# Kernel tuning notes

Measured on AMD Instinct MI355X. Metric: run time of the kernel, lower is better.

The kernel has to match this reference:

```python
import jax, jax.numpy as jnp
import numpy as np

N_NODES = 100000
N_EDGES = 3200000
D = 16
L = 3


def setup_inputs() -> dict:
    key = jax.random.key(0)
    ks = jax.random.split(key, 7)
    scale = 1.0 / np.sqrt(D)
    x = jax.random.normal(ks[0], (N_NODES, D), dtype=jnp.float32)
    edge_index = jax.random.randint(ks[1], (2, N_EDGES), 0, N_NODES, dtype=jnp.int64)
    Wl = jax.random.normal(ks[2], (L, D, D), dtype=jnp.float32) * scale
    bl = jax.random.normal(ks[3], (L, D), dtype=jnp.float32) * scale
    Wr = jax.random.normal(ks[4], (L, D, D), dtype=jnp.float32) * scale
    Wlin = jax.random.normal(ks[5], (L, D, D), dtype=jnp.float32) * scale
    blin = jax.random.normal(ks[6], (L, D), dtype=jnp.float32) * scale
    return {"x": x, "edge_index": edge_index, "Wl": Wl, "bl": bl,
            "Wr": Wr, "Wlin": Wlin, "blin": blin}


def reference(x, edge_index, Wl, bl, Wr, Wlin, blin):
    src = edge_index[0]
    dst = edge_index[1]
    n = x.shape[0]
    # in-degree for mean aggregation (PyG SAGEConv aggr='mean')
    deg = jax.ops.segment_sum(jnp.ones((src.shape[0],), dtype=x.dtype), dst,
                              num_segments=n)
    denom = jnp.maximum(deg, 1.0)[:, None]  # nodes with no in-edges -> 0 agg
    for i in range(Wl.shape[0]):
        # gather source features, scatter-mean onto targets
        agg = jax.ops.segment_sum(x[src], dst, num_segments=n) / denom
        conv = agg @ Wl[i].T + bl[i] + x @ Wr[i].T  # SAGEConv: lin_l(agg)+lin_r(x)
        x = conv + x @ Wlin[i].T + blin[i]          # + Linear residual
    return x
```

## Files before the change

kernel.cpp:

```cpp
#include <hip/hip_runtime.h>

#define N_NODES 100000
#define N_EDGES 3200000
#define D 16

#define TILE 128
#define NB ((N_NODES + TILE - 1) / TILE)
#define CAP 4608
#define NBLK 500
#define SEG (N_EDGES / NBLK)
#define BINT 1024
#define CVTB 391
#define LT 512
#define N4 (N_NODES * D / 4)

__device__ __forceinline__ unsigned packbf(float a, float b) {
    unsigned ua = __float_as_uint(a); ua += 0x7FFFu + ((ua >> 16) & 1u);
    unsigned ub = __float_as_uint(b); ub += 0x7FFFu + ((ub >> 16) & 1u);
    return (ua >> 16) | (ub & 0xFFFF0000u);
}
#define BLO(u) __uint_as_float((u) << 16)
#define BHI(u) __uint_as_float((u) & 0xFFFF0000u)

__global__ __launch_bounds__(BINT, 8) void pre_kernel(
        const float* __restrict__ x, unsigned* __restrict__ xbf,
        const int* __restrict__ src, const int* __restrict__ dst,
        int* __restrict__ cursor, unsigned* __restrict__ ebuf) {
    __shared__ int lcnt[NB];
    __shared__ int ldiff[NB];
    __shared__ unsigned sorted[SEG];
    __shared__ unsigned short sbkt[SEG];
    __shared__ int wsum[16];
    int tid = threadIdx.x;

    if (blockIdx.x >= NBLK) {
        int t = (blockIdx.x - NBLK) * BINT + tid;
        if (t < N4) {
            float4 v = *(const float4*)(x + (size_t)t * 4);
            uint2 o; o.x = packbf(v.x, v.y); o.y = packbf(v.z, v.w);
            *(uint2*)(xbf + (size_t)t * 2) = o;
        }
        return;
    }

    for (int i = tid; i < NB; i += BINT) lcnt[i] = 0;
    __syncthreads();
    int b0 = blockIdx.x * SEG;
    for (int e = b0 + tid * 4; e < b0 + SEG; e += BINT * 4) {
        int4 d4 = *(const int4*)(dst + e);
        atomicAdd(&lcnt[d4.x >> 7], 1);
        atomicAdd(&lcnt[d4.y >> 7], 1);
        atomicAdd(&lcnt[d4.z >> 7], 1);
        atomicAdd(&lcnt[d4.w >> 7], 1);
    }
    __syncthreads();
    {
        int lane = tid & 63, wv = tid >> 6;
        int v = (tid < NB) ? lcnt[tid] : 0;
        int s = v;
        #pragma unroll
        for (int d_ = 1; d_ < 64; d_ <<= 1) {
            int u = __shfl_up(s, d_, 64);
            if (lane >= d_) s += u;
        }
        if (lane == 63) wsum[wv] = s;
        __syncthreads();
        if (tid == 0) {
            int a = 0;
            #pragma unroll
            for (int i = 0; i < 16; i++) { int t_ = wsum[i]; wsum[i] = a; a += t_; }
        }
        __syncthreads();
        int excl = wsum[wv] + s - v;
        if (tid < NB) {
            int g = v ? (tid * CAP + atomicAdd(&cursor[tid], v)) : 0;
            ldiff[tid] = g - excl;
            lcnt[tid] = excl;
        }
        __syncthreads();
    }
    for (int e = b0 + tid * 4; e < b0 + SEG; e += BINT * 4) {
        int4 d4 = *(const int4*)(dst + e);
        int4 s4 = *(const int4*)(src + e);
        int b_, pos;
        b_ = d4.x >> 7; pos = atomicAdd(&lcnt[b_], 1);
        sorted[pos] = ((unsigned)(d4.x & 127) << 17) | (unsigned)s4.x; sbkt[pos] = (unsigned short)b_;
        b_ = d4.y >> 7; pos = atomicAdd(&lcnt[b_], 1);
        sorted[pos] = ((unsigned)(d4.y & 127) << 17) | (unsigned)s4.y; sbkt[pos] = (unsigned short)b_;
        b_ = d4.z >> 7; pos = atomicAdd(&lcnt[b_], 1);
        sorted[pos] = ((unsigned)(d4.z & 127) << 17) | (unsigned)s4.z; sbkt[pos] = (unsigned short)b_;
        b_ = d4.w >> 7; pos = atomicAdd(&lcnt[b_], 1);
        sorted[pos] = ((unsigned)(d4.w & 127) << 17) | (unsigned)s4.w; sbkt[pos] = (unsigned short)b_;
    }
    __syncthreads();
    for (int i = tid; i < SEG; i += BINT) {
        int b_ = sbkt[i];
        ebuf[ldiff[b_] + i] = sorted[i];
    }
}

#define LDG(j) (*(const uint4*)(xbf + (size_t)(se2[(j) + lane2] & 0x1FFFF) * 8 + ho))
#define LDC(j) (*(const uint4*)(xbf + (size_t)(se2[min((j) + lane2, s1m1)] & 0x1FFFF) * 8 + ho))
#define ACC8(g) do { \
    acc[0] += BLO((g).x); acc[1] += BHI((g).x); acc[2] += BLO((g).y); acc[3] += BHI((g).y); \
    acc[4] += BLO((g).z); acc[5] += BHI((g).z); acc[6] += BLO((g).w); acc[7] += BHI((g).w); } while (0)
#define ACC8M(g, m) do { \
    acc[0] = fmaf((m), BLO((g).x), acc[0]); acc[1] = fmaf((m), BHI((g).x), acc[1]); \
    acc[2] = fmaf((m), BLO((g).y), acc[2]); acc[3] = fmaf((m), BHI((g).y), acc[3]); \
    acc[4] = fmaf((m), BLO((g).z), acc[4]); acc[5] = fmaf((m), BHI((g).z), acc[5]); \
    acc[6] = fmaf((m), BLO((g).w), acc[6]); acc[7] = fmaf((m), BHI((g).w), acc[7]); } while (0)

__device__ __forceinline__ void agg_xform(
    const float* __restrict__ xin, const unsigned* __restrict__ xbf,
    const unsigned* se2, const int* lofs, int n_loc,
    const float* sWl, const float* sWc, const float* sbc,
    float* __restrict__ xout, unsigned* __restrict__ xbf_out,
    int emit_bf, int b, int N, int tid) {
    int q = tid & 3;
    int n = b * TILE + n_loc;
    if (n >= N) return;

    float4 xq = *(const float4*)(xin + (size_t)n * D + q * 4);
    float xv[4] = { xq.x, xq.y, xq.z, xq.w };

    int s0 = lofs[n_loc];
    int s1 = lofs[n_loc + 1];
    int deg = s1 - s0;
    int lane2 = q >> 1;
    int ho = (q & 1) * 4;

    float acc[8] = {0.f,0.f,0.f,0.f,0.f,0.f,0.f,0.f};
    int end8 = s0 + (deg & ~7);
    int i = s0;
    if (i < end8) {
        uint4 c0 = LDG(i + 0), c1 = LDG(i + 2), c2 = LDG(i + 4), c3 = LDG(i + 6);
        i += 8;
        for (; i < end8; i += 8) {
            uint4 n0 = LDG(i + 0), n1 = LDG(i + 2), n2 = LDG(i + 4), n3 = LDG(i + 6);
            ACC8(c0); ACC8(c1); ACC8(c2); ACC8(c3);
            c0 = n0; c1 = n1; c2 = n2; c3 = n3;
        }
        ACC8(c0); ACC8(c1); ACC8(c2); ACC8(c3);
    }
    if (i < s1) {
        int s1m1 = s1 - 1;
        int j0 = i + lane2;
        float m0 = (j0 + 0 < s1) ? 1.f : 0.f;
        float m1 = (j0 + 2 < s1) ? 1.f : 0.f;
        float m2 = (j0 + 4 < s1) ? 1.f : 0.f;
        float m3 = (j0 + 6 < s1) ? 1.f : 0.f;
        uint4 e0 = LDC(i + 0), e1 = LDC(i + 2), e2 = LDC(i + 4), e3 = LDC(i + 6);
        ACC8M(e0, m0); ACC8M(e1, m1); ACC8M(e2, m2); ACC8M(e3, m3);
    }
    #pragma unroll
    for (int k = 0; k < 8; k++) acc[k] += __shfl_xor(acc[k], 2, 4);

    int srcAbs = (tid & 63 & ~3) | (q >> 1);
    float inv = 1.0f / fmaxf((float)deg, 1.0f);
    float a[4];
    #pragma unroll
    for (int k = 0; k < 4; k++) {
        float lo = __shfl(acc[k], srcAbs);
        float hi = __shfl(acc[4 + k], srcAbs);
        a[k] = ((q & 1) ? hi : lo) * inv;
    }

    float o[4];
    #pragma unroll
    for (int j = 0; j < D; j++) {
        float p = 0.f;
        #pragma unroll
        for (int k = 0; k < 4; k++) {
            int kk = q * 4 + k;
            p += a[k] * sWl[j * D + kk] + xv[k] * sWc[j * D + kk];
        }
        p += __shfl_xor(p, 1, 4);
        p += __shfl_xor(p, 2, 4);
        if ((j >> 2) == q) o[j & 3] = p + sbc[j];
    }
    *(float4*)(xout + (size_t)n * D + q * 4) = make_float4(o[0], o[1], o[2], o[3]);
    if (emit_bf) {
        uint2 ob; ob.x = packbf(o[0], o[1]); ob.y = packbf(o[2], o[3]);
        *(uint2*)(xbf_out + (size_t)n * 8 + q * 2) = ob;
    }
}

__global__ void layer0_kernel(
        const float* __restrict__ xin, const unsigned* __restrict__ xbf,
        unsigned* __restrict__ ebuf, const int* __restrict__ cnt,
        int* __restrict__ node_start, int* __restrict__ gperm,
        const float* __restrict__ Wl, const float* __restrict__ bl,
        const float* __restrict__ Wr, const float* __restrict__ Wlin,
        const float* __restrict__ blin,
        float* __restrict__ xout, unsigned* __restrict__ xbf_out, int N) {
    __shared__ unsigned se[CAP];
    __shared__ unsigned se2[CAP];
    __shared__ int lcnt[TILE];
    __shared__ int lofs[TILE + 1];
    __shared__ int sdeg[TILE];
    __shared__ int perm[TILE];
    __shared__ float sWl[D * D];
    __shared__ float sWc[D * D];
    __shared__ float sbc[D];

    int tid = threadIdx.x;
    int b = blockIdx.x;
    int base = b * CAP;
    int nE = min(cnt[b], CAP);
    int nE4 = (nE + 3) >> 2;

    if (tid < D * D) { sWl[tid] = Wl[tid]; sWc[tid] = Wr[tid] + Wlin[tid]; }
    if (tid < D) sbc[tid] = bl[tid] + blin[tid];
    if (tid < TILE) lcnt[tid] = 0;
    for (int i = tid; i < nE4; i += LT)
        ((uint4*)se)[i] = ((const uint4*)(ebuf + base))[i];
    __syncthreads();
    for (int i = tid; i < nE; i += LT)
        atomicAdd(&lcnt[se[i] >> 17], 1);
    __syncthreads();
    if (tid < 64) {
        int l2 = tid * 2;
        int c0 = lcnt[l2], c1 = lcnt[l2 + 1];
        int v = c0 + c1, s = v;
        #pragma unroll
        for (int d_ = 1; d_ < 64; d_ <<= 1) {
            int u = __shfl_up(s, d_, 64);
            if (tid >= d_) s += u;
        }
        int excl = s - v;
        lofs[l2] = excl; sdeg[l2] = c0; lcnt[l2] = excl;
        node_start[b * TILE + l2] = excl;
        int e1 = excl + c0;
        lofs[l2 + 1] = e1; sdeg[l2 + 1] = c1; lcnt[l2 + 1] = e1;
        node_start[b * TILE + l2 + 1] = e1;
        if (tid == 63) lofs[TILE] = s;
    }
    __syncthreads();
    if (tid < TILE) {
        int dm = sdeg[tid];
        int r = 0;
        for (int j = 0; j < TILE; j++) {
            int dj = sdeg[j];
            r += (dj > dm) || (dj == dm && j < tid);
        }
        perm[r] = tid;
        gperm[b * TILE + r] = tid;
    }
    for (int i = tid; i < nE; i += LT) {
        unsigned p = se[i];
        int pos = atomicAdd(&lcnt[p >> 17], 1);
        se2[pos] = p;
    }
    __syncthreads();
    for (int i = tid; i < nE4; i += LT)
        ((uint4*)(ebuf + base))[i] = ((const uint4*)se2)[i];

    agg_xform(xin, xbf, se2, lofs, perm[tid >> 2], sWl, sWc, sbc,
              xout, xbf_out, 1, b, N, tid);
}

__global__ __launch_bounds__(LT, 8) void layerN_kernel(
        const float* __restrict__ xin, const unsigned* __restrict__ xbf,
        const unsigned* __restrict__ ebuf, const int* __restrict__ cnt,
        const int* __restrict__ node_start, const int* __restrict__ gperm,
        const float* __restrict__ Wl, const float* __restrict__ bl,
        const float* __restrict__ Wr, const float* __restrict__ Wlin,
        const float* __restrict__ blin,
        float* __restrict__ xout, unsigned* __restrict__ xbf_out,
        int emit_bf, int N) {
    __shared__ unsigned se2[CAP];
    __shared__ int lofs[TILE + 1];
    __shared__ float sWl[D * D];
    __shared__ float sWc[D * D];
    __shared__ float sbc[D];

    int tid = threadIdx.x;
    int b = blockIdx.x;
    int base = b * CAP;
    int nE = min(cnt[b], CAP);
    int nE4 = (nE + 3) >> 2;

    if (tid < D * D) { sWl[tid] = Wl[tid]; sWc[tid] = Wr[tid] + Wlin[tid]; }
    if (tid < D) sbc[tid] = bl[tid] + blin[tid];
    if (tid < TILE) lofs[tid] = node_start[b * TILE + tid];
    if (tid == 0) lofs[TILE] = nE;
    for (int i = tid; i < nE4; i += LT)
        ((uint4*)se2)[i] = ((const uint4*)(ebuf + base))[i];
    int n_loc = gperm[b * TILE + (tid >> 2)];
    __syncthreads();

    agg_xform(xin, xbf, se2, lofs, n_loc, sWl, sWc, sbc,
              xout, xbf_out, emit_bf, b, N, tid);
}

extern "C" void kernel_launch(void* const* d_in, const int* in_sizes, int n_in,
                              void* d_out, int out_size, void* d_ws, size_t ws_size,
                              hipStream_t stream) {
    const float* x    = (const float*)d_in[0];
    const int*   ei   = (const int*)d_in[1];
    const float* Wl   = (const float*)d_in[2];
    const float* bl   = (const float*)d_in[3];
    const float* Wr   = (const float*)d_in[4];
    const float* Wlin = (const float*)d_in[5];
    const float* blin = (const float*)d_in[6];
    float* out = (float*)d_out;

    const int* src = ei;
    const int* dst = ei + N_EDGES;

    char* w = (char*)d_ws;
    unsigned* ebuf   = (unsigned*)w;  w += (size_t)NB * CAP * 4;
    float* bufA      = (float*)w;     w += (size_t)N_NODES * D * 4;
    float* bufB      = (float*)w;     w += (size_t)N_NODES * D * 4;
    unsigned* xbf0   = (unsigned*)w;  w += (size_t)N_NODES * 8 * 4;
    unsigned* xbf1   = (unsigned*)w;  w += (size_t)N_NODES * 8 * 4;
    int*   cursor    = (int*)w;       w += (size_t)NB * 4;
    int*   node_start= (int*)w;       w += (size_t)NB * TILE * 4;
    int*   gperm     = (int*)w;       w += (size_t)NB * TILE * 4;

    hipMemsetAsync(cursor, 0, (size_t)NB * 4, stream);
    pre_kernel<<<NBLK + CVTB, BINT, 0, stream>>>(x, xbf0, src, dst, cursor, ebuf);

    layer0_kernel<<<NB, LT, 0, stream>>>(
        x, xbf0, ebuf, cursor, node_start, gperm,
        Wl, bl, Wr, Wlin, blin, bufA, xbf1, N_NODES);
    layerN_kernel<<<NB, LT, 0, stream>>>(
        bufA, xbf1, ebuf, cursor, node_start, gperm,
        Wl + D * D, bl + D, Wr + D * D, Wlin + D * D, blin + D, bufB, xbf0, 1, N_NODES);
    layerN_kernel<<<NB, LT, 0, stream>>>(
        bufB, xbf0, ebuf, cursor, node_start, gperm,
        Wl + 2 * D * D, bl + 2 * D, Wr + 2 * D * D, Wlin + 2 * D * D, blin + 2 * D,
        out, nullptr, 0, N_NODES);
}
```

Baseline: 188.9 us.

## Halve node tile to 64, fold bf16 conversion into bucketing blocks, drop layer0 staging buffer

Shrinks the destination-node tile from 128 to 64 nodes, which doubles the bucket count to 1563 and cuts per-block edge capacity and threads to 256. The pre-kernel scan now handles two buckets per thread, and the separate bf16-conversion blocks are merged into the 500 bucketing blocks. layer0 reads edges straight from global memory twice instead of staging them in a second shared array, halving its shared memory. The smaller blocks should raise occupancy and balance load, at the cost of more blocks and a higher overflow risk from the tighter CAP.

```diff
diff --git a/kernel.cpp b/kernel.cpp
--- a/kernel.cpp
+++ b/kernel.cpp
@@ -4,14 +4,13 @@
 #define N_EDGES 3200000
 #define D 16
 
-#define TILE 128
+#define TILE 64
 #define NB ((N_NODES + TILE - 1) / TILE)
-#define CAP 4608
+#define CAP 2432
 #define NBLK 500
 #define SEG (N_EDGES / NBLK)
 #define BINT 1024
-#define CVTB 391
-#define LT 512
+#define LT 256
 #define N4 (N_NODES * D / 4)
 
 __device__ __forceinline__ unsigned packbf(float a, float b) {
@@ -33,14 +32,13 @@
     __shared__ int wsum[16];
     int tid = threadIdx.x;
 
-    if (blockIdx.x >= NBLK) {
-        int t = (blockIdx.x - NBLK) * BINT + tid;
+    {
+        int t = blockIdx.x * BINT + tid;
         if (t < N4) {
             float4 v = *(const float4*)(x + (size_t)t * 4);
             uint2 o; o.x = packbf(v.x, v.y); o.y = packbf(v.z, v.w);
             *(uint2*)(xbf + (size_t)t * 2) = o;
         }
-        return;
     }
 
     for (int i = tid; i < NB; i += BINT) lcnt[i] = 0;
@@ -48,16 +46,18 @@
     int b0 = blockIdx.x * SEG;
     for (int e = b0 + tid * 4; e < b0 + SEG; e += BINT * 4) {
         int4 d4 = *(const int4*)(dst + e);
-        atomicAdd(&lcnt[d4.x >> 7], 1);
-        atomicAdd(&lcnt[d4.y >> 7], 1);
-        atomicAdd(&lcnt[d4.z >> 7], 1);
-        atomicAdd(&lcnt[d4.w >> 7], 1);
+        atomicAdd(&lcnt[d4.x >> 6], 1);
+        atomicAdd(&lcnt[d4.y >> 6], 1);
+        atomicAdd(&lcnt[d4.z >> 6], 1);
+        atomicAdd(&lcnt[d4.w >> 6], 1);
     }
     __syncthreads();
     {
         int lane = tid & 63, wv = tid >> 6;
-        int v = (tid < NB) ? lcnt[tid] : 0;
-        int s = v;
+        int i2 = tid * 2;
+        int c0 = (i2 < NB) ? lcnt[i2] : 0;
+        int c1 = (i2 + 1 < NB) ? lcnt[i2 + 1] : 0;
+        int v = c0 + c1, s = v;
         #pragma unroll
         for (int d_ = 1; d_ < 64; d_ <<= 1) {
             int u = __shfl_up(s, d_, 64);
@@ -72,10 +72,16 @@
         }
         __syncthreads();
         int excl = wsum[wv] + s - v;
-        if (tid < NB) {
-            int g = v ? (tid * CAP + atomicAdd(&cursor[tid], v)) : 0;
-            ldiff[tid] = g - excl;
-            lcnt[tid] = excl;
+        if (i2 < NB) {
+            int g = c0 ? (i2 * CAP + atomicAdd(&cursor[i2], c0)) : 0;
+            ldiff[i2] = g - excl;
+            lcnt[i2] = excl;
+        }
+        if (i2 + 1 < NB) {
+            int e1 = excl + c0;
+            int g = c1 ? ((i2 + 1) * CAP + atomicAdd(&cursor[i2 + 1], c1)) : 0;
+            ldiff[i2 + 1] = g - e1;
+            lcnt[i2 + 1] = e1;
         }
         __syncthreads();
     }
@@ -83,14 +89,14 @@
         int4 d4 = *(const int4*)(dst + e);
         int4 s4 = *(const int4*)(src + e);
         int b_, pos;
-        b_ = d4.x >> 7; pos = atomicAdd(&lcnt[b_], 1);
-        sorted[pos] = ((unsigned)(d4.x & 127) << 17) | (unsigned)s4.x; sbkt[pos] = (unsigned short)b_;
-        b_ = d4.y >> 7; pos = atomicAdd(&lcnt[b_], 1);
-        sorted[pos] = ((unsigned)(d4.y & 127) << 17) | (unsigned)s4.y; sbkt[pos] = (unsigned short)b_;
-        b_ = d4.z >> 7; pos = atomicAdd(&lcnt[b_], 1);
-        sorted[pos] = ((unsigned)(d4.z & 127) << 17) | (unsigned)s4.z; sbkt[pos] = (unsigned short)b_;
-        b_ = d4.w >> 7; pos = atomicAdd(&lcnt[b_], 1);
-        sorted[pos] = ((unsigned)(d4.w & 127) << 17) | (unsigned)s4.w; sbkt[pos] = (unsigned short)b_;
+        b_ = d4.x >> 6; pos = atomicAdd(&lcnt[b_], 1);
+        sorted[pos] = ((unsigned)(d4.x & 63) << 17) | (unsigned)s4.x; sbkt[pos] = (unsigned short)b_;
+        b_ = d4.y >> 6; pos = atomicAdd(&lcnt[b_], 1);
+        sorted[pos] = ((unsigned)(d4.y & 63) << 17) | (unsigned)s4.y; sbkt[pos] = (unsigned short)b_;
+        b_ = d4.z >> 6; pos = atomicAdd(&lcnt[b_], 1);
+        sorted[pos] = ((unsigned)(d4.z & 63) << 17) | (unsigned)s4.z; sbkt[pos] = (unsigned short)b_;
+        b_ = d4.w >> 6; pos = atomicAdd(&lcnt[b_], 1);
+        sorted[pos] = ((unsigned)(d4.w & 63) << 17) | (unsigned)s4.w; sbkt[pos] = (unsigned short)b_;
     }
     __syncthreads();
     for (int i = tid; i < SEG; i += BINT) {
@@ -185,7 +191,7 @@
     }
 }
 
-__global__ void layer0_kernel(
+__global__ __launch_bounds__(LT, 8) void layer0_kernel(
         const float* __restrict__ xin, const unsigned* __restrict__ xbf,
         unsigned* __restrict__ ebuf, const int* __restrict__ cnt,
         int* __restrict__ node_start, int* __restrict__ gperm,
@@ -193,7 +199,6 @@
         const float* __restrict__ Wr, const float* __restrict__ Wlin,
         const float* __restrict__ blin,
         float* __restrict__ xout, unsigned* __restrict__ xbf_out, int N) {
-    __shared__ unsigned se[CAP];
     __shared__ unsigned se2[CAP];
     __shared__ int lcnt[TILE];
     __shared__ int lofs[TILE + 1];
@@ -212,18 +217,22 @@
     if (tid < D * D) { sWl[tid] = Wl[tid]; sWc[tid] = Wr[tid] + Wlin[tid]; }
     if (tid < D) sbc[tid] = bl[tid] + blin[tid];
     if (tid < TILE) lcnt[tid] = 0;
-    for (int i = tid; i < nE4; i += LT)
-        ((uint4*)se)[i] = ((const uint4*)(ebuf + base))[i];
-    __syncthreads();
-    for (int i = tid; i < nE; i += LT)
-        atomicAdd(&lcnt[se[i] >> 17], 1);
-    __syncthreads();
-    if (tid < 64) {
+    __syncthreads();
+    for (int i4 = tid; i4 < nE4; i4 += LT) {
+        uint4 qv = ((const uint4*)(ebuf + base))[i4];
+        int k0 = i4 * 4;
+        if (k0 < nE)     atomicAdd(&lcnt[qv.x >> 17], 1);
+        if (k0 + 1 < nE) atomicAdd(&lcnt[qv.y >> 17], 1);
+        if (k0 + 2 < nE) atomicAdd(&lcnt[qv.z >> 17], 1);
+        if (k0 + 3 < nE) atomicAdd(&lcnt[qv.w >> 17], 1);
+    }
+    __syncthreads();
+    if (tid < 32) {
         int l2 = tid * 2;
         int c0 = lcnt[l2], c1 = lcnt[l2 + 1];
         int v = c0 + c1, s = v;
         #pragma unroll
-        for (int d_ = 1; d_ < 64; d_ <<= 1) {
+        for (int d_ = 1; d_ < 32; d_ <<= 1) {
             int u = __shfl_up(s, d_, 64);
             if (tid >= d_) s += u;
         }
@@ -233,7 +242,7 @@
         int e1 = excl + c0;
         lofs[l2 + 1] = e1; sdeg[l2 + 1] = c1; lcnt[l2 + 1] = e1;
         node_start[b * TILE + l2 + 1] = e1;
-        if (tid == 63) lofs[TILE] = s;
+        if (tid == 31) lofs[TILE] = s;
     }
     __syncthreads();
     if (tid < TILE) {
@@ -246,14 +255,17 @@
         perm[r] = tid;
         gperm[b * TILE + r] = tid;
     }
-    for (int i = tid; i < nE; i += LT) {
-        unsigned p = se[i];
-        int pos = atomicAdd(&lcnt[p >> 17], 1);
-        se2[pos] = p;
-    }
-    __syncthreads();
-    for (int i = tid; i < nE4; i += LT)
-        ((uint4*)(ebuf + base))[i] = ((const uint4*)se2)[i];
+    for (int i4 = tid; i4 < nE4; i4 += LT) {
+        uint4 qv = ((const uint4*)(ebuf + base))[i4];
+        int k0 = i4 * 4;
+        if (k0 < nE)     { int pos = atomicAdd(&lcnt[qv.x >> 17], 1); se2[pos] = qv.x; }
+        if (k0 + 1 < nE) { int pos = atomicAdd(&lcnt[qv.y >> 17], 1); se2[pos] = qv.y; }
+        if (k0 + 2 < nE) { int pos = atomicAdd(&lcnt[qv.z >> 17], 1); se2[pos] = qv.z; }
+        if (k0 + 3 < nE) { int pos = atomicAdd(&lcnt[qv.w >> 17], 1); se2[pos] = qv.w; }
+    }
+    __syncthreads();
+    for (int i4 = tid; i4 < nE4; i4 += LT)
+        ((uint4*)(ebuf + base))[i4] = ((const uint4*)se2)[i4];
 
     agg_xform(xin, xbf, se2, lofs, perm[tid >> 2], sWl, sWc, sbc,
               xout, xbf_out, 1, b, N, tid);
@@ -318,8 +330,8 @@
     int*   node_start= (int*)w;       w += (size_t)NB * TILE * 4;
     int*   gperm     = (int*)w;       w += (size_t)NB * TILE * 4;
 
-    hipMemsetAsync(cursor, 0, (size_t)NB * 4, stream);
-    pre_kernel<<<NBLK + CVTB, BINT, 0, stream>>>(x, xbf0, src, dst, cursor, ebuf);
+    (void)hipMemsetAsync(cursor, 0, (size_t)NB * 4, stream);
+    pre_kernel<<<NBLK, BINT, 0, stream>>>(x, xbf0, src, dst, cursor, ebuf);
 
     layer0_kernel<<<NB, LT, 0, stream>>>(
         x, xbf0, ebuf, cursor, node_start, gperm,
```

After: 195.1 us. +3.3%, slower.
